# Optimization experiments

Hardware: AMD Instinct MI355X
Metric: run time of the kernel (lower is better)

Reference implementation:

```python
import jax, jax.numpy as jnp
import numpy as np

N_NODES = 100000
N_EDGES = 1200000
IN_CH = 128
HID = 256
OUT_CH = 64
N_ETYPES = 8
N_DIFF = 1000


def setup_inputs() -> dict:
    key = jax.random.key(0)
    ks = jax.random.split(key, 20)
    s = 0.05
    inp = {
        'x': jax.random.normal(ks[0], (N_NODES, IN_CH), jnp.float32),
        'edge_index': jax.random.randint(ks[1], (2, N_EDGES), 0, N_NODES, jnp.int64),
        'edge_type': jax.random.randint(ks[2], (N_EDGES,), 0, N_ETYPES, jnp.int64),
        'diff_idx': jax.random.randint(ks[3], (N_DIFF,), 0, N_NODES, jnp.int64),
        # lin: in_ch -> hid -> out_ch
        'lin1_w': jax.random.normal(ks[4], (HID, IN_CH), jnp.float32) * s,
        'lin1_b': jnp.zeros((HID,), jnp.float32),
        'lin2_w': jax.random.normal(ks[5], (OUT_CH, HID), jnp.float32) * s,
        'lin2_b': jnp.zeros((OUT_CH,), jnp.float32),
        # GRUCell(out_ch, out_ch): gates ordered r, z, n as in torch
        'gru_w_ih': jax.random.normal(ks[6], (3 * OUT_CH, OUT_CH), jnp.float32) * s,
        'gru_w_hh': jax.random.normal(ks[7], (3 * OUT_CH, OUT_CH), jnp.float32) * s,
        'gru_b_ih': jnp.zeros((3 * OUT_CH,), jnp.float32),
        'gru_b_hh': jnp.zeros((3 * OUT_CH,), jnp.float32),
        'edge_type_weight': jax.random.normal(ks[8], (N_ETYPES,), jnp.float32),
        # fc: out_ch -> hid -> 2
        'fc1_w': jax.random.normal(ks[9], (HID, OUT_CH), jnp.float32) * s,
        'fc1_b': jnp.zeros((HID,), jnp.float32),
        'fc2_w': jax.random.normal(ks[10], (2, HID), jnp.float32) * s,
        'fc2_b': jnp.zeros((2,), jnp.float32),
        'w_imp': jnp.float32(1.0),
    }
    return inp


def _gru_cell(m, h, w_ih, w_hh, b_ih, b_hh):
    # torch GRUCell: gates [r, z, n]
    gi = m @ w_ih.T + b_ih  # [N, 3H]
    gh = h @ w_hh.T + b_hh
    gi_r, gi_z, gi_n = jnp.split(gi, 3, axis=-1)
    gh_r, gh_z, gh_n = jnp.split(gh, 3, axis=-1)
    r = jax.nn.sigmoid(gi_r + gh_r)
    z = jax.nn.sigmoid(gi_z + gh_z)
    n = jnp.tanh(gi_n + r * gh_n)
    return (1.0 - z) * n + z * h


def reference(x, edge_index, edge_type, diff_idx,
              lin1_w, lin1_b, lin2_w, lin2_b,
              gru_w_ih, gru_w_hh, gru_b_ih, gru_b_hh,
              edge_type_weight,
              fc1_w, fc1_b, fc2_w, fc2_b, w_imp):
    N = x.shape[0]
    src, dst = edge_index[0], edge_index[1]
    # input projection MLP
    h = jax.nn.relu(x @ lin1_w.T + lin1_b) @ lin2_w.T + lin2_b  # [N, OUT]
    # per-edge softplus weight (constant across iterations)
    w_e = jax.nn.softplus(edge_type_weight[edge_type])[:, None]  # [E, 1]
    # degree for mean aggregation (isolated nodes -> 0 message)
    deg = jax.ops.segment_sum(jnp.ones_like(src, dtype=h.dtype), dst, num_segments=N)
    deg = jnp.maximum(deg, 1.0)[:, None]
    for _ in range(3):
        msg = w_e * h[src]  # gather + weight, [E, OUT]
        m = jax.ops.segment_sum(msg, dst, num_segments=N) / deg  # scatter-mean
        h = _gru_cell(m, h, gru_w_ih, gru_w_hh, gru_b_ih, gru_b_hh)
    # importance-weighted global pooling
    w_pos = jax.nn.softplus(w_imp)
    alpha = jnp.ones((N, 1), h.dtype).at[diff_idx].set(1.0 + w_pos)
    pooled = (alpha * h).sum(axis=0, keepdims=True) / alpha.sum()  # [1, OUT]
    out = jax.nn.relu(pooled @ fc1_w.T + fc1_b) @ fc2_w.T + fc2_b  # [1, 2]
    return jax.nn.log_softmax(out, axis=1)
```

## Files before the change

kernel.cpp:

```cpp
#include <hip/hip_runtime.h>
#include <math.h>

#define NN 100000
#define NE 1200000
#define NDIFF 1000
#define CAP 48
#define SLICE 2048
#define NQ 200
#define SUBN 500
#define QCAPB 32
#define NSH 8
#define SQS 1024

typedef short short8 __attribute__((ext_vector_type(8)));
typedef float floatx4 __attribute__((ext_vector_type(4)));
typedef float floatx2 __attribute__((ext_vector_type(2)));
typedef unsigned short ushort_t;
typedef unsigned long long ull_t;

__device__ __forceinline__ float softplusf_(float x) {
  return fmaxf(x, 0.f) + logf(1.f + __expf(-fabsf(x)));
}
__device__ __forceinline__ float sigmoidf_(float x) {
  return 1.f / (1.f + __expf(-x));
}
__device__ __forceinline__ float tanhf_fast(float x) {
  float ax = fabsf(x);
  float e = __expf(-2.f * ax);
  float t = (1.f - e) / (1.f + e);
  return x < 0.f ? -t : t;
}
__device__ __forceinline__ ushort_t f2bf(float f) {
  unsigned u = __float_as_uint(f);
  unsigned r = (u + 0x7FFFu + ((u >> 16) & 1u)) >> 16;
  return (ushort_t)r;
}
__device__ __forceinline__ float bf2f(ushort_t s) {
  return __uint_as_float(((unsigned)s) << 16);
}
__device__ __forceinline__ uint2 bf8_to_fp8x8(short8 v) {
  float f[8];
  #pragma unroll
  for (int i = 0; i < 8; ++i) f[i] = bf2f((ushort_t)v[i]);
  int a = 0, b = 0;
  a = __builtin_amdgcn_cvt_pk_fp8_f32(f[0], f[1], a, false);
  a = __builtin_amdgcn_cvt_pk_fp8_f32(f[2], f[3], a, true);
  b = __builtin_amdgcn_cvt_pk_fp8_f32(f[4], f[5], b, false);
  b = __builtin_amdgcn_cvt_pk_fp8_f32(f[6], f[7], b, true);
  uint2 r; r.x = (unsigned)a; r.y = (unsigned)b;
  return r;
}


__global__ void prep_w_kernel(const float* __restrict__ lin1_w, const float* __restrict__ lin2_w,
                              const float* __restrict__ w_ih, const float* __restrict__ w_hh,
                              const float* __restrict__ etw, const int* __restrict__ diff,
                              ushort_t* __restrict__ W1s, ushort_t* __restrict__ W2s,
                              ushort_t* __restrict__ Wcs, float* __restrict__ wtab,
                              unsigned char* __restrict__ flagb) {
  int i = blockIdx.x * 256 + threadIdx.x;
  if (i < 8) wtab[i] = softplusf_(etw[i]);
  if (i < NDIFF) flagb[diff[i]] = 1;
  if (i < 32768) {
    int fi = i >> 9, lane = (i >> 3) & 63, j = i & 7;
    int s = fi >> 4, ct = fi & 15;
    int quad = lane >> 4, l15 = lane & 15;
    int col = ct * 16 + l15, k = s * 32 + quad * 8 + j;
    W1s[i] = f2bf(lin1_w[col * 128 + k]);
  } else if (i < 49152) {
    int i2 = i - 32768;
    int fi = i2 >> 9, lane = (i2 >> 3) & 63, j = i2 & 7;
    int s = fi >> 2, ct = fi & 3;
    int quad = lane >> 4, l15 = lane & 15;
    int col = ct * 16 + l15, k = s * 32 + quad * 8 + j;
    W2s[i2] = f2bf(lin2_w[col * 256 + k]);
  } else {
    int i3 = i - 49152;
    int fi = i3 >> 9, lane = (i3 >> 3) & 63, j = i3 & 7;
    int s = fi >> 4, ct = fi & 15;
    int quad = lane >> 4, l15 = lane & 15;
    int jj = ct * 16 + l15, k = s * 32 + quad * 8 + j;
    float v;
    if (jj < 128)      v = (k < 64) ? w_ih[jj * 64 + k] : w_hh[jj * 64 + (k - 64)];
    else if (jj < 192) v = (k < 64) ? w_ih[jj * 64 + k] : 0.f;
    else               v = (k < 64) ? 0.f : w_hh[(jj - 64) * 64 + (k - 64)];
    Wcs[i3] = f2bf(v);
  }
}


__launch_bounds__(256)
__global__ void bin_kernel(const int* __restrict__ src, const int* __restrict__ dst,
                           const int* __restrict__ etype,
                           unsigned* __restrict__ gtail, ull_t* __restrict__ staging) {
  __shared__ uint2 bin[NQ][QCAPB];
  __shared__ unsigned lcur[NQ];
  int t = threadIdx.x;
  int shard = blockIdx.x & 7;
  for (int i = t; i < NQ; i += 256) lcur[i] = 0;
  __syncthreads();
  int base = blockIdx.x * SLICE;

  uint2 rec[8];
  int qq[8];
  unsigned idx[8];
  #pragma unroll
  for (int it = 0; it < 8; ++it) {
    int e = base + it * 256 + t;
    qq[it] = -1;
    if (e < NE) {
      int d = __builtin_nontemporal_load(&dst[e]);
      int s = __builtin_nontemporal_load(&src[e]);
      int tv = __builtin_nontemporal_load(&etype[e]);
      rec[it].x = (unsigned)(s | (tv << 17));
      rec[it].y = (unsigned)d;
      int q = d / SUBN;
      qq[it] = q;
      unsigned i = atomicAdd(&lcur[q], 1u);
      idx[it] = i;
      if (i < QCAPB) bin[q][i] = rec[it];
    }
  }
  __syncthreads();
  if (t < NQ) {
    unsigned c = min(lcur[t], (unsigned)QCAPB);
    if (c) {
      unsigned gb = atomicAdd(&gtail[(t * NSH + shard) * 16], c);
      ull_t* qst = staging + (size_t)(t * NSH + shard) * SQS + gb;
      const uint2* b = bin[t];
      for (unsigned i = 0; i < c; ++i)
        qst[i] = ((ull_t)b[i].y << 32) | (ull_t)b[i].x;
    }
  }
  #pragma unroll
  for (int it = 0; it < 8; ++it) {
    if (qq[it] >= 0 && idx[it] >= QCAPB) {
      unsigned gb = atomicAdd(&gtail[(qq[it] * NSH + shard) * 16], 1u);
      staging[(size_t)(qq[it] * NSH + shard) * SQS + gb] =
          ((ull_t)rec[it].y << 32) | (ull_t)rec[it].x;
    }
  }
}

__launch_bounds__(512)
__global__ void scatter_kernel(const ull_t* __restrict__ staging,
                               const unsigned* __restrict__ gtail,
                               unsigned* __restrict__ cpack, int* __restrict__ csr) {
  __shared__ int cnt[SUBN];
  int t = threadIdx.x;
  int q = blockIdx.x;
  int n0 = q * SUBN;
  for (int i = t; i < SUBN; i += 512) cnt[i] = 0;
  __syncthreads();

  #pragma unroll 1
  for (int sh = 0; sh < NSH; ++sh) {
    unsigned n = gtail[(q * NSH + sh) * 16];
    const ull_t* st = staging + (size_t)(q * NSH + sh) * SQS;
    for (unsigned i = t; i < n; i += 512) {
      ull_t r = st[i];
      int d = (int)(r >> 32);
      int rank = atomicAdd(&cnt[d - n0], 1);
      csr[d * CAP + rank] = (int)(unsigned)r;
    }
  }
  __syncthreads();

  if (t < SUBN / 4) {
    unsigned w = (unsigned)cnt[t * 4] | ((unsigned)cnt[t * 4 + 1] << 8) |
                 ((unsigned)cnt[t * 4 + 2] << 16) | ((unsigned)cnt[t * 4 + 3] << 24);
    cpack[(n0 >> 2) + t] = w;
  }
}


__launch_bounds__(256)
__global__ void mlp_kernel(const float* __restrict__ x,
                           const ushort_t* __restrict__ W1s, const float* __restrict__ b1,
                           const ushort_t* __restrict__ W2s, const float* __restrict__ b2,
                           ushort_t* __restrict__ mh, unsigned char* __restrict__ h8) {
  __shared__ ushort_t S[64 * 264];
  int t = threadIdx.x;
  int wv = t >> 6, lane = t & 63;
  int quad = lane >> 4, l15 = lane & 15;
  int nb = blockIdx.x * 64;

  #pragma unroll
  for (int it = 0; it < 8; ++it) {
    int f = it * 256 + t;
    int row = f >> 5, off4 = f & 31;
    int grow = min(nb + row, NN - 1);
    float4 v = *(const float4*)&x[(size_t)grow * 128 + off4 * 4];
    union { uint2 d; ushort_t u[4]; } pk;
    pk.u[0] = f2bf(v.x); pk.u[1] = f2bf(v.y); pk.u[2] = f2bf(v.z); pk.u[3] = f2bf(v.w);
    *(uint2*)&S[row * 136 + off4 * 4] = pk.d;
  }
  __syncthreads();

  floatx4 acc1[4][4];
  #pragma unroll
  for (int rt = 0; rt < 4; ++rt)
    #pragma unroll
    for (int c = 0; c < 4; ++c) acc1[rt][c] = (floatx4)0.f;

  #pragma unroll
  for (int s = 0; s < 4; ++s) {
    short8 av[4];
    #pragma unroll
    for (int rt = 0; rt < 4; ++rt)
      av[rt] = *(const short8*)&S[(rt * 16 + l15) * 136 + s * 32 + quad * 8];
    #pragma unroll
    for (int c = 0; c < 4; ++c) {
      short8 bv = *(const short8*)&W1s[((s * 16 + wv * 4 + c) * 64 + lane) * 8];
      #pragma unroll
      for (int rt = 0; rt < 4; ++rt)
        acc1[rt][c] = __builtin_amdgcn_mfma_f32_16x16x32_bf16(av[rt], bv, acc1[rt][c], 0, 0, 0);
    }
  }
  __syncthreads();

  #pragma unroll
  for (int c = 0; c < 4; ++c) {
    int col = (wv * 4 + c) * 16 + l15;
    float bb = b1[col];
    #pragma unroll
    for (int rt = 0; rt < 4; ++rt)
      #pragma unroll
      for (int reg = 0; reg < 4; ++reg)
        S[(rt * 16 + quad * 4 + reg) * 264 + col] = f2bf(fmaxf(acc1[rt][c][reg] + bb, 0.f));
  }
  __syncthreads();

  floatx4 acc2[4];
  #pragma unroll
  for (int c = 0; c < 4; ++c) acc2[c] = (floatx4)0.f;
  #pragma unroll
  for (int s = 0; s < 8; ++s) {
    short8 av = *(const short8*)&S[(wv * 16 + l15) * 264 + s * 32 + quad * 8];
    #pragma unroll
    for (int c = 0; c < 4; ++c) {
      short8 bv = *(const short8*)&W2s[((s * 4 + c) * 64 + lane) * 8];
      acc2[c] = __builtin_amdgcn_mfma_f32_16x16x32_bf16(av, bv, acc2[c], 0, 0, 0);
    }
  }
  __syncthreads();

  #pragma unroll
  for (int c = 0; c < 4; ++c) {
    int col = c * 16 + l15;
    float bb = b2[c * 16 + l15];
    #pragma unroll
    for (int reg = 0; reg < 4; ++reg)
      S[(wv * 16 + quad * 4 + reg) * 72 + col] = f2bf(acc2[c][reg] + bb);
  }
  __syncthreads();

  #pragma unroll
  for (int it = 0; it < 2; ++it) {
    int idx = it * 256 + t;
    int row = idx >> 3, ch = idx & 7;
    int node = nb + row;
    if (node < NN) {
      short8 v = *(const short8*)&S[row * 72 + ch * 8];
      *(short8*)&mh[(size_t)node * 64 + ch * 8] = v;
      *(uint2*)&h8[(size_t)node * 64 + ch * 8] = bf8_to_fp8x8(v);
    }
  }
}


__launch_bounds__(256, 8)
__global__ void agru_kernel(const ushort_t* __restrict__ mhin,
                            const unsigned char* __restrict__ h8in,
                            const unsigned* __restrict__ cpack,
                            const int* __restrict__ csr, const float* __restrict__ wtab,
                            const ushort_t* __restrict__ Wcs,
                            const float* __restrict__ b_ih, const float* __restrict__ b_hh,
                            ushort_t* __restrict__ mhout, unsigned char* __restrict__ h8out) {
  __shared__ ushort_t As[32 * 136];
  __shared__ ushort_t Os[32 * 72];
  __shared__ float wt[16];
  int t = threadIdx.x;
  int nb = blockIdx.x * 32;
  if (t < 16) wt[t] = (t < 8) ? wtab[t] : 0.f;
  __syncthreads();

  int g8 = t >> 3, lane8 = t & 7;
  int node = nb + g8;

  short8 hreg = *(const short8*)&mhin[(size_t)node * 64 + lane8 * 8];

  int deg = (cpack[node >> 2] >> ((node & 3) * 8)) & 255;
  int s = node * CAP;
  float f0 = 0.f, f1 = 0.f, f2 = 0.f, f3 = 0.f;
  float f4 = 0.f, f5 = 0.f, f6 = 0.f, f7 = 0.f;
  for (int p = 0; p < deg; p += 8) {
    int k[8];
    uint2 v[8];
    #pragma unroll
    for (int i = 0; i < 8; ++i) {
      int q = p + i;
      k[i] = (q < deg) ? __builtin_nontemporal_load(&csr[s + q]) : (8 << 17);
    }
    #pragma unroll
    for (int i = 0; i < 8; ++i)
      v[i] = *(const uint2*)&h8in[(size_t)(k[i] & 0x1FFFF) * 64 + lane8 * 8];
    #pragma unroll
    for (int i = 0; i < 8; ++i) {
      float w = wt[k[i] >> 17];
      floatx2 xlo = __builtin_amdgcn_cvt_pk_f32_fp8((int)v[i].x, false);
      floatx2 xhi = __builtin_amdgcn_cvt_pk_f32_fp8((int)v[i].x, true);
      floatx2 ylo = __builtin_amdgcn_cvt_pk_f32_fp8((int)v[i].y, false);
      floatx2 yhi = __builtin_amdgcn_cvt_pk_f32_fp8((int)v[i].y, true);
      f0 += w * xlo[0]; f1 += w * xlo[1]; f2 += w * xhi[0]; f3 += w * xhi[1];
      f4 += w * ylo[0]; f5 += w * ylo[1]; f6 += w * yhi[0]; f7 += w * yhi[1];
    }
  }
  {
    float invd = 1.f / fmaxf((float)deg, 1.f);
    short8 pk;
    pk[0] = (short)f2bf(f0 * invd); pk[1] = (short)f2bf(f1 * invd);
    pk[2] = (short)f2bf(f2 * invd); pk[3] = (short)f2bf(f3 * invd);
    pk[4] = (short)f2bf(f4 * invd); pk[5] = (short)f2bf(f5 * invd);
    pk[6] = (short)f2bf(f6 * invd); pk[7] = (short)f2bf(f7 * invd);
    *(short8*)&As[g8 * 136 + lane8 * 8] = pk;
    *(short8*)&As[g8 * 136 + 64 + lane8 * 8] = hreg;
  }
  __syncthreads();

  int wv = t >> 6, lane = t & 63;
  int quad = lane >> 4, l15 = lane & 15;

  floatx4 acc[2][4];
  #pragma unroll
  for (int rt = 0; rt < 2; ++rt)
    #pragma unroll
    for (int g = 0; g < 4; ++g) acc[rt][g] = (floatx4)0.f;

  #pragma unroll
  for (int s4 = 0; s4 < 4; ++s4) {
    short8 av[2];
    #pragma unroll
    for (int rt = 0; rt < 2; ++rt)
      av[rt] = *(const short8*)&As[(rt * 16 + l15) * 136 + s4 * 32 + quad * 8];
    #pragma unroll
    for (int g = 0; g < 4; ++g) {
      short8 bv = *(const short8*)&Wcs[((s4 * 16 + g * 4 + wv) * 64 + lane) * 8];
      #pragma unroll
      for (int rt = 0; rt < 2; ++rt)
        acc[rt][g] = __builtin_amdgcn_mfma_f32_16x16x32_bf16(av[rt], bv, acc[rt][g], 0, 0, 0);
    }
  }

  int j = wv * 16 + l15;
  float bir = b_ih[j] + b_hh[j];
  float biz = b_ih[64 + j] + b_hh[64 + j];
  float bin_ = b_ih[128 + j];
  float bhn = b_hh[128 + j];
  #pragma unroll
  for (int rt = 0; rt < 2; ++rt) {
    #pragma unroll
    for (int reg = 0; reg < 4; ++reg) {
      int lrow = rt * 16 + quad * 4 + reg;
      float r = sigmoidf_(acc[rt][0][reg] + bir);
      float z = sigmoidf_(acc[rt][1][reg] + biz);
      float n = tanhf_fast(acc[rt][2][reg] + bin_ + r * (acc[rt][3][reg] + bhn));
      float hp = bf2f(As[lrow * 136 + 64 + j]);
      Os[lrow * 72 + j] = f2bf((1.f - z) * n + z * hp);
    }
  }
  __syncthreads();

  {
    short8 v = *(const short8*)&Os[g8 * 72 + lane8 * 8];
    *(short8*)&mhout[(size_t)node * 64 + lane8 * 8] = v;
    *(uint2*)&h8out[(size_t)node * 64 + lane8 * 8] = bf8_to_fp8x8(v);
  }
}


__global__ void pool_kernel(const ushort_t* __restrict__ mh, const unsigned char* __restrict__ flag,
                            float* __restrict__ pooled) {
  int gw = (blockIdx.x * 256 + threadIdx.x) >> 6;
  int lane = threadIdx.x & 63;
  const int chunk = (NN + 1023) / 1024;
  int n0 = gw * chunk;
  int n1 = min(n0 + chunk, NN);
  float base = 0.f, fl = 0.f, cnt = 0.f;
  int n = n0;
  for (; n + 4 <= n1; n += 4) {
    float v0 = bf2f(mh[(size_t)(n + 0) * 64 + lane]);
    float v1 = bf2f(mh[(size_t)(n + 1) * 64 + lane]);
    float v2 = bf2f(mh[(size_t)(n + 2) * 64 + lane]);
    float v3 = bf2f(mh[(size_t)(n + 3) * 64 + lane]);
    int f0 = flag[n + 0], f1 = flag[n + 1], f2 = flag[n + 2], f3 = flag[n + 3];
    base += (v0 + v1) + (v2 + v3);
    if (f0) { fl += v0; cnt += 1.f; }
    if (f1) { fl += v1; cnt += 1.f; }
    if (f2) { fl += v2; cnt += 1.f; }
    if (f3) { fl += v3; cnt += 1.f; }
  }
  for (; n < n1; ++n) {
    float v = bf2f(mh[(size_t)n * 64 + lane]);
    base += v;
    if (flag[n]) { fl += v; cnt += 1.f; }
  }
  atomicAdd(&pooled[lane], base);
  atomicAdd(&pooled[64 + lane], fl);
  if (lane == 0) atomicAdd(&pooled[128], cnt);
}

__global__ void final_kernel(const float* __restrict__ pooled,
                             const float* __restrict__ fc1_w, const float* __restrict__ fc1_b,
                             const float* __restrict__ fc2_w, const float* __restrict__ fc2_b,
                             const float* __restrict__ w_imp, float* __restrict__ out) {
  __shared__ float p[64];
  __shared__ float hid[256];
  __shared__ float o[2];
  int t = threadIdx.x;
  float wpos = softplusf_(w_imp[0]);
  if (t < 64) {
    float num = pooled[t] + wpos * pooled[64 + t];
    float den = (float)NN + wpos * pooled[128];
    p[t] = num / den;
  }
  __syncthreads();
  {
    float a = 0.f;
    for (int k = 0; k < 64; ++k) a += p[k] * fc1_w[t * 64 + k];
    hid[t] = fmaxf(a + fc1_b[t], 0.f);
  }
  __syncthreads();
  if (t < 2) {
    float a = 0.f;
    for (int k = 0; k < 256; ++k) a += hid[k] * fc2_w[t * 256 + k];
    o[t] = a + fc2_b[t];
  }
  __syncthreads();
  if (t == 0) {
    float mx = fmaxf(o[0], o[1]);
    float lse = mx + logf(__expf(o[0] - mx) + __expf(o[1] - mx));
    out[0] = o[0] - lse;
    out[1] = o[1] - lse;
  }
}


extern "C" void kernel_launch(void* const* d_in, const int* in_sizes, int n_in,
                              void* d_out, int out_size, void* d_ws, size_t ws_size,
                              hipStream_t stream) {
  const float* x        = (const float*)d_in[0];
  const int*   ei       = (const int*)d_in[1];
  const int*   etype    = (const int*)d_in[2];
  const int*   diff_idx = (const int*)d_in[3];
  const float* lin1_w   = (const float*)d_in[4];
  const float* lin1_b   = (const float*)d_in[5];
  const float* lin2_w   = (const float*)d_in[6];
  const float* lin2_b   = (const float*)d_in[7];
  const float* gru_w_ih = (const float*)d_in[8];
  const float* gru_w_hh = (const float*)d_in[9];
  const float* gru_b_ih = (const float*)d_in[10];
  const float* gru_b_hh = (const float*)d_in[11];
  const float* etw      = (const float*)d_in[12];
  const float* fc1_w    = (const float*)d_in[13];
  const float* fc1_b    = (const float*)d_in[14];
  const float* fc2_w    = (const float*)d_in[15];
  const float* fc2_b    = (const float*)d_in[16];
  const float* w_imp    = (const float*)d_in[17];
  float* out = (float*)d_out;

  char* ws = (char*)d_ws;
  size_t off = 0;
  auto alloc = [&](size_t bytes) -> void* {
    void* p = ws + off;
    off += (bytes + 255) & ~(size_t)255;
    return p;
  };
  ushort_t* mh0   = (ushort_t*)alloc((size_t)NN * 64 * 2);
  ushort_t* mh1   = (ushort_t*)alloc((size_t)NN * 64 * 2);
  unsigned char* h8a = (unsigned char*)alloc((size_t)NN * 64);
  unsigned char* h8b = (unsigned char*)alloc((size_t)NN * 64);
  int*   csr      = (int*)  alloc((size_t)NN * CAP * 4);
  ull_t* staging  = (ull_t*)alloc((size_t)NQ * NSH * SQS * 8);
  ushort_t* W1s   = (ushort_t*)alloc(128 * 256 * 2);
  ushort_t* W2s   = (ushort_t*)alloc(256 * 64 * 2);
  ushort_t* Wcs   = (ushort_t*)alloc(128 * 256 * 2);
  float* wtab     = (float*)alloc(8 * 4);
  const size_t gtb = (size_t)NQ * NSH * 16 * 4;
  char* zbase     = (char*)alloc(gtb + (size_t)NN + NN + 129 * 4);
  unsigned* gtail = (unsigned*)zbase;
  unsigned* cpack = (unsigned*)(zbase + gtb);
  unsigned char* flagb = (unsigned char*)(zbase + gtb + NN);
  float* pooled   = (float*)(zbase + gtb + NN + NN);
  const size_t zbytes = gtb + (size_t)NN + NN + 129 * 4;

  const int ngemm = (NN + 63) / 64;
  const int nagru = NN / 32;
  const int nbin  = (NE + SLICE - 1) / SLICE;

  hipMemsetAsync(zbase, 0, zbytes, stream);
  prep_w_kernel<<<320, 256, 0, stream>>>(lin1_w, lin2_w, gru_w_ih, gru_w_hh, etw, diff_idx,
                                         W1s, W2s, Wcs, wtab, flagb);
  bin_kernel<<<nbin, 256, 0, stream>>>(ei, ei + NE, etype, gtail, staging);
  scatter_kernel<<<NQ, 512, 0, stream>>>(staging, gtail, cpack, csr);
  mlp_kernel<<<ngemm, 256, 0, stream>>>(x, W1s, lin1_b, W2s, lin2_b, mh0, h8a);

  agru_kernel<<<nagru, 256, 0, stream>>>(mh0, h8a, cpack, csr, wtab, Wcs,
                                         gru_b_ih, gru_b_hh, mh1, h8b);
  agru_kernel<<<nagru, 256, 0, stream>>>(mh1, h8b, cpack, csr, wtab, Wcs,
                                         gru_b_ih, gru_b_hh, mh0, h8a);
  agru_kernel<<<nagru, 256, 0, stream>>>(mh0, h8a, cpack, csr, wtab, Wcs,
                                         gru_b_ih, gru_b_hh, mh1, h8b);

  pool_kernel<<<256, 256, 0, stream>>>(mh1, flagb, pooled);
  final_kernel<<<1, 256, 0, stream>>>(pooled, fc1_w, fc1_b, fc2_w, fc2_b, w_imp, out);
}
```

Baseline: 351.0 us.

## Fuse three GRU rounds and pooling into one cooperative persistent kernel

Replaces the three agru launches and the pool kernel with a single cooperative kernel. Each block owns 64 nodes, keeps its hidden state in registers across rounds, and uses grid.sync between rounds. Only the fp8 copy is written back, and pooling runs in-block with shared-memory atomics. This removes the launch gaps, the bf16 hidden-state writes and reads, and the separate pool pass. In exchange it adds grid-wide barriers and requires all 1563 blocks to be co-resident, which limits occupancy and makes the slowest block gate each round.

```diff
diff --git a/kernel.cpp b/kernel.cpp
--- a/kernel.cpp
+++ b/kernel.cpp
@@ -1,5 +1,8 @@
 #include <hip/hip_runtime.h>
+#include <hip/hip_cooperative_groups.h>
 #include <math.h>
+
+namespace cg = cooperative_groups;
 
 #define NN 100000
 #define NE 1200000
@@ -11,6 +14,7 @@
 #define QCAPB 32
 #define NSH 8
 #define SQS 1024
+#define PB 1563
 
 typedef short short8 __attribute__((ext_vector_type(8)));
 typedef float floatx4 __attribute__((ext_vector_type(4)));
@@ -270,145 +274,163 @@
 
 
 __launch_bounds__(256, 8)
-__global__ void agru_kernel(const ushort_t* __restrict__ mhin,
-                            const unsigned char* __restrict__ h8in,
-                            const unsigned* __restrict__ cpack,
-                            const int* __restrict__ csr, const float* __restrict__ wtab,
-                            const ushort_t* __restrict__ Wcs,
-                            const float* __restrict__ b_ih, const float* __restrict__ b_hh,
-                            ushort_t* __restrict__ mhout, unsigned char* __restrict__ h8out) {
+__global__ void agru3_kernel(const ushort_t* __restrict__ mh0,
+                             unsigned char* __restrict__ h8a,
+                             unsigned char* __restrict__ h8b,
+                             const unsigned* __restrict__ cpack,
+                             const int* __restrict__ csr, const float* __restrict__ wtab,
+                             const ushort_t* __restrict__ Wcs,
+                             const float* __restrict__ b_ih, const float* __restrict__ b_hh,
+                             const unsigned char* __restrict__ flagb,
+                             float* __restrict__ pooled) {
   __shared__ ushort_t As[32 * 136];
   __shared__ ushort_t Os[32 * 72];
   __shared__ float wt[16];
+  __shared__ float red[129];
   int t = threadIdx.x;
-  int nb = blockIdx.x * 32;
+  int nb = blockIdx.x * 64;
   if (t < 16) wt[t] = (t < 8) ? wtab[t] : 0.f;
-  __syncthreads();
+  for (int i = t; i < 129; i += 256) red[i] = 0.f;
 
   int g8 = t >> 3, lane8 = t & 7;
-  int node = nb + g8;
-
-  short8 hreg = *(const short8*)&mhin[(size_t)node * 64 + lane8 * 8];
-
-  int deg = (cpack[node >> 2] >> ((node & 3) * 8)) & 255;
-  int s = node * CAP;
-  float f0 = 0.f, f1 = 0.f, f2 = 0.f, f3 = 0.f;
-  float f4 = 0.f, f5 = 0.f, f6 = 0.f, f7 = 0.f;
-  for (int p = 0; p < deg; p += 8) {
-    int k[8];
-    uint2 v[8];
-    #pragma unroll
-    for (int i = 0; i < 8; ++i) {
-      int q = p + i;
-      k[i] = (q < deg) ? __builtin_nontemporal_load(&csr[s + q]) : (8 << 17);
-    }
-    #pragma unroll
-    for (int i = 0; i < 8; ++i)
-      v[i] = *(const uint2*)&h8in[(size_t)(k[i] & 0x1FFFF) * 64 + lane8 * 8];
-    #pragma unroll
-    for (int i = 0; i < 8; ++i) {
-      float w = wt[k[i] >> 17];
-      floatx2 xlo = __builtin_amdgcn_cvt_pk_f32_fp8((int)v[i].x, false);
-      floatx2 xhi = __builtin_amdgcn_cvt_pk_f32_fp8((int)v[i].x, true);
-      floatx2 ylo = __builtin_amdgcn_cvt_pk_f32_fp8((int)v[i].y, false);
-      floatx2 yhi = __builtin_amdgcn_cvt_pk_f32_fp8((int)v[i].y, true);
-      f0 += w * xlo[0]; f1 += w * xlo[1]; f2 += w * xhi[0]; f3 += w * xhi[1];
-      f4 += w * ylo[0]; f5 += w * ylo[1]; f6 += w * yhi[0]; f7 += w * yhi[1];
-    }
-  }
-  {
-    float invd = 1.f / fmaxf((float)deg, 1.f);
-    short8 pk;
-    pk[0] = (short)f2bf(f0 * invd); pk[1] = (short)f2bf(f1 * invd);
-    pk[2] = (short)f2bf(f2 * invd); pk[3] = (short)f2bf(f3 * invd);
-    pk[4] = (short)f2bf(f4 * invd); pk[5] = (short)f2bf(f5 * invd);
-    pk[6] = (short)f2bf(f6 * invd); pk[7] = (short)f2bf(f7 * invd);
-    *(short8*)&As[g8 * 136 + lane8 * 8] = pk;
-    *(short8*)&As[g8 * 136 + 64 + lane8 * 8] = hreg;
-  }
-  __syncthreads();
-
   int wv = t >> 6, lane = t & 63;
   int quad = lane >> 4, l15 = lane & 15;
 
-  floatx4 acc[2][4];
-  #pragma unroll
-  for (int rt = 0; rt < 2; ++rt)
-    #pragma unroll
-    for (int g = 0; g < 4; ++g) acc[rt][g] = (floatx4)0.f;
-
-  #pragma unroll
-  for (int s4 = 0; s4 < 4; ++s4) {
-    short8 av[2];
-    #pragma unroll
-    for (int rt = 0; rt < 2; ++rt)
-      av[rt] = *(const short8*)&As[(rt * 16 + l15) * 136 + s4 * 32 + quad * 8];
-    #pragma unroll
-    for (int g = 0; g < 4; ++g) {
-      short8 bv = *(const short8*)&Wcs[((s4 * 16 + g * 4 + wv) * 64 + lane) * 8];
-      #pragma unroll
-      for (int rt = 0; rt < 2; ++rt)
-        acc[rt][g] = __builtin_amdgcn_mfma_f32_16x16x32_bf16(av[rt], bv, acc[rt][g], 0, 0, 0);
-    }
-  }
-
+  short8 hreg0, hreg1;
+  {
+    int n0 = min(nb + g8, NN - 1);
+    int n1 = min(nb + 32 + g8, NN - 1);
+    hreg0 = *(const short8*)&mh0[(size_t)n0 * 64 + lane8 * 8];
+    hreg1 = *(const short8*)&mh0[(size_t)n1 * 64 + lane8 * 8];
+  }
   int j = wv * 16 + l15;
   float bir = b_ih[j] + b_hh[j];
   float biz = b_ih[64 + j] + b_hh[64 + j];
   float bin_ = b_ih[128 + j];
   float bhn = b_hh[128 + j];
-  #pragma unroll
-  for (int rt = 0; rt < 2; ++rt) {
-    #pragma unroll
-    for (int reg = 0; reg < 4; ++reg) {
-      int lrow = rt * 16 + quad * 4 + reg;
-      float r = sigmoidf_(acc[rt][0][reg] + bir);
-      float z = sigmoidf_(acc[rt][1][reg] + biz);
-      float n = tanhf_fast(acc[rt][2][reg] + bin_ + r * (acc[rt][3][reg] + bhn));
-      float hp = bf2f(As[lrow * 136 + 64 + j]);
-      Os[lrow * 72 + j] = f2bf((1.f - z) * n + z * hp);
-    }
-  }
-  __syncthreads();
-
-  {
-    short8 v = *(const short8*)&Os[g8 * 72 + lane8 * 8];
-    *(short8*)&mhout[(size_t)node * 64 + lane8 * 8] = v;
-    *(uint2*)&h8out[(size_t)node * 64 + lane8 * 8] = bf8_to_fp8x8(v);
-  }
-}
-
-
-__global__ void pool_kernel(const ushort_t* __restrict__ mh, const unsigned char* __restrict__ flag,
-                            float* __restrict__ pooled) {
-  int gw = (blockIdx.x * 256 + threadIdx.x) >> 6;
-  int lane = threadIdx.x & 63;
-  const int chunk = (NN + 1023) / 1024;
-  int n0 = gw * chunk;
-  int n1 = min(n0 + chunk, NN);
-  float base = 0.f, fl = 0.f, cnt = 0.f;
-  int n = n0;
-  for (; n + 4 <= n1; n += 4) {
-    float v0 = bf2f(mh[(size_t)(n + 0) * 64 + lane]);
-    float v1 = bf2f(mh[(size_t)(n + 1) * 64 + lane]);
-    float v2 = bf2f(mh[(size_t)(n + 2) * 64 + lane]);
-    float v3 = bf2f(mh[(size_t)(n + 3) * 64 + lane]);
-    int f0 = flag[n + 0], f1 = flag[n + 1], f2 = flag[n + 2], f3 = flag[n + 3];
-    base += (v0 + v1) + (v2 + v3);
-    if (f0) { fl += v0; cnt += 1.f; }
-    if (f1) { fl += v1; cnt += 1.f; }
-    if (f2) { fl += v2; cnt += 1.f; }
-    if (f3) { fl += v3; cnt += 1.f; }
-  }
-  for (; n < n1; ++n) {
-    float v = bf2f(mh[(size_t)n * 64 + lane]);
-    base += v;
-    if (flag[n]) { fl += v; cnt += 1.f; }
-  }
-  atomicAdd(&pooled[lane], base);
-  atomicAdd(&pooled[64 + lane], fl);
-  if (lane == 0) atomicAdd(&pooled[128], cnt);
-}
+
+  cg::grid_group grid = cg::this_grid();
+  __syncthreads();
+
+  unsigned char* h8cur = h8a;
+  unsigned char* h8nxt = h8b;
+
+  #pragma unroll 1
+  for (int r = 0; r < 3; ++r) {
+    #pragma unroll
+    for (int tl = 0; tl < 2; ++tl) {
+      short8 hin = tl ? hreg1 : hreg0;
+      int node = nb + tl * 32 + g8;
+      bool valid = node < NN;
+      int deg = 0;
+      if (valid) deg = (cpack[node >> 2] >> ((node & 3) * 8)) & 255;
+      int sbase = node * CAP;
+      float f0 = 0.f, f1 = 0.f, f2 = 0.f, f3 = 0.f;
+      float f4 = 0.f, f5 = 0.f, f6 = 0.f, f7 = 0.f;
+      for (int p = 0; p < deg; p += 8) {
+        int k[8];
+        uint2 v[8];
+        #pragma unroll
+        for (int i = 0; i < 8; ++i) {
+          int q = p + i;
+          k[i] = (q < deg) ? __builtin_nontemporal_load(&csr[sbase + q]) : (8 << 17);
+        }
+        #pragma unroll
+        for (int i = 0; i < 8; ++i)
+          v[i] = *(const uint2*)&h8cur[(size_t)(k[i] & 0x1FFFF) * 64 + lane8 * 8];
+        #pragma unroll
+        for (int i = 0; i < 8; ++i) {
+          float w = wt[k[i] >> 17];
+          floatx2 xlo = __builtin_amdgcn_cvt_pk_f32_fp8((int)v[i].x, false);
+          floatx2 xhi = __builtin_amdgcn_cvt_pk_f32_fp8((int)v[i].x, true);
+          floatx2 ylo = __builtin_amdgcn_cvt_pk_f32_fp8((int)v[i].y, false);
+          floatx2 yhi = __builtin_amdgcn_cvt_pk_f32_fp8((int)v[i].y, true);
+          f0 += w * xlo[0]; f1 += w * xlo[1]; f2 += w * xhi[0]; f3 += w * xhi[1];
+          f4 += w * ylo[0]; f5 += w * ylo[1]; f6 += w * yhi[0]; f7 += w * yhi[1];
+        }
+      }
+      __syncthreads();
+      {
+        float invd = 1.f / fmaxf((float)deg, 1.f);
+        short8 pk;
+        pk[0] = (short)f2bf(f0 * invd); pk[1] = (short)f2bf(f1 * invd);
+        pk[2] = (short)f2bf(f2 * invd); pk[3] = (short)f2bf(f3 * invd);
+        pk[4] = (short)f2bf(f4 * invd); pk[5] = (short)f2bf(f5 * invd);
+        pk[6] = (short)f2bf(f6 * invd); pk[7] = (short)f2bf(f7 * invd);
+        *(short8*)&As[g8 * 136 + lane8 * 8] = pk;
+        *(short8*)&As[g8 * 136 + 64 + lane8 * 8] = hin;
+      }
+      __syncthreads();
+
+      floatx4 acc[2][4];
+      #pragma unroll
+      for (int rt = 0; rt < 2; ++rt)
+        #pragma unroll
+        for (int g = 0; g < 4; ++g) acc[rt][g] = (floatx4)0.f;
+
+      #pragma unroll
+      for (int s4 = 0; s4 < 4; ++s4) {
+        short8 av[2];
+        #pragma unroll
+        for (int rt = 0; rt < 2; ++rt)
+          av[rt] = *(const short8*)&As[(rt * 16 + l15) * 136 + s4 * 32 + quad * 8];
+        #pragma unroll
+        for (int g = 0; g < 4; ++g) {
+          short8 bv = *(const short8*)&Wcs[((s4 * 16 + g * 4 + wv) * 64 + lane) * 8];
+          #pragma unroll
+          for (int rt = 0; rt < 2; ++rt)
+            acc[rt][g] = __builtin_amdgcn_mfma_f32_16x16x32_bf16(av[rt], bv, acc[rt][g], 0, 0, 0);
+        }
+      }
+
+      #pragma unroll
+      for (int rt = 0; rt < 2; ++rt) {
+        #pragma unroll
+        for (int reg = 0; reg < 4; ++reg) {
+          int lrow = rt * 16 + quad * 4 + reg;
+          float rr = sigmoidf_(acc[rt][0][reg] + bir);
+          float z = sigmoidf_(acc[rt][1][reg] + biz);
+          float n = tanhf_fast(acc[rt][2][reg] + bin_ + rr * (acc[rt][3][reg] + bhn));
+          float hp = bf2f(As[lrow * 136 + 64 + j]);
+          Os[lrow * 72 + j] = f2bf((1.f - z) * n + z * hp);
+        }
+      }
+      __syncthreads();
+
+      {
+        short8 vo = *(const short8*)&Os[g8 * 72 + lane8 * 8];
+        if (tl) hreg1 = vo; else hreg0 = vo;
+        if (valid && r < 2)
+          *(uint2*)&h8nxt[(size_t)node * 64 + lane8 * 8] = bf8_to_fp8x8(vo);
+      }
+    }
+    if (r < 2) {
+      grid.sync();
+      unsigned char* tmp = h8cur; h8cur = h8nxt; h8nxt = tmp;
+    }
+  }
+
+  __syncthreads();
+  #pragma unroll
+  for (int tl = 0; tl < 2; ++tl) {
+    short8 hv = tl ? hreg1 : hreg0;
+    int node = nb + tl * 32 + g8;
+    bool valid = node < NN;
+    int fb = valid ? (int)flagb[node] : 0;
+    if (valid) {
+      #pragma unroll
+      for (int c = 0; c < 8; ++c) {
+        float val = bf2f((ushort_t)hv[c]);
+        atomicAdd(&red[lane8 * 8 + c], val);
+        if (fb) atomicAdd(&red[64 + lane8 * 8 + c], val);
+      }
+      if (fb && lane8 == 0) atomicAdd(&red[128], 1.f);
+    }
+  }
+  __syncthreads();
+  if (t < 129) atomicAdd(&pooled[t], red[t]);
+}
+
 
 __global__ void final_kernel(const float* __restrict__ pooled,
                              const float* __restrict__ fc1_w, const float* __restrict__ fc1_b,
@@ -477,7 +499,6 @@
     return p;
   };
   ushort_t* mh0   = (ushort_t*)alloc((size_t)NN * 64 * 2);
-  ushort_t* mh1   = (ushort_t*)alloc((size_t)NN * 64 * 2);
   unsigned char* h8a = (unsigned char*)alloc((size_t)NN * 64);
   unsigned char* h8b = (unsigned char*)alloc((size_t)NN * 64);
   int*   csr      = (int*)  alloc((size_t)NN * CAP * 4);
@@ -495,7 +516,6 @@
   const size_t zbytes = gtb + (size_t)NN + NN + 129 * 4;
 
   const int ngemm = (NN + 63) / 64;
-  const int nagru = NN / 32;
   const int nbin  = (NE + SLICE - 1) / SLICE;
 
   hipMemsetAsync(zbase, 0, zbytes, stream);
@@ -505,13 +525,24 @@
   scatter_kernel<<<NQ, 512, 0, stream>>>(staging, gtail, cpack, csr);
   mlp_kernel<<<ngemm, 256, 0, stream>>>(x, W1s, lin1_b, W2s, lin2_b, mh0, h8a);
 
-  agru_kernel<<<nagru, 256, 0, stream>>>(mh0, h8a, cpack, csr, wtab, Wcs,
-                                         gru_b_ih, gru_b_hh, mh1, h8b);
-  agru_kernel<<<nagru, 256, 0, stream>>>(mh1, h8b, cpack, csr, wtab, Wcs,
-                                         gru_b_ih, gru_b_hh, mh0, h8a);
-  agru_kernel<<<nagru, 256, 0, stream>>>(mh0, h8a, cpack, csr, wtab, Wcs,
-                                         gru_b_ih, gru_b_hh, mh1, h8b);
-
-  pool_kernel<<<256, 256, 0, stream>>>(mh1, flagb, pooled);
+  {
+    const ushort_t* a_mh0 = mh0;
+    unsigned char* a_h8a = h8a;
+    unsigned char* a_h8b = h8b;
+    const unsigned* a_cpack = cpack;
+    const int* a_csr = csr;
+    const float* a_wtab = wtab;
+    const ushort_t* a_Wcs = Wcs;
+    const float* a_bih = gru_b_ih;
+    const float* a_bhh = gru_b_hh;
+    const unsigned char* a_flag = flagb;
+    float* a_pooled = pooled;
+    void* args[] = {(void*)&a_mh0, (void*)&a_h8a, (void*)&a_h8b, (void*)&a_cpack,
+                    (void*)&a_csr, (void*)&a_wtab, (void*)&a_Wcs, (void*)&a_bih,
+                    (void*)&a_bhh, (void*)&a_flag, (void*)&a_pooled};
+    hipLaunchCooperativeKernel((const void*)agru3_kernel, dim3(PB), dim3(256),
+                               args, 0, stream);
+  }
+
   final_kernel<<<1, 256, 0, stream>>>(pooled, fc1_w, fc1_b, fc2_w, fc2_b, w_imp, out);
 }
```

New measurement: 946.3 us. 2.7x slower.
